# Performance work log

Hardware: AMD Instinct MI355X
Metric: run time of the kernel (lower is better)

Reference implementation:

```python
import jax, jax.numpy as jnp
import numpy as np

B, N, IN, H = 8, 2048, 256, 128
ALPHA = 0.2  # leaky relu slope


def setup_inputs() -> dict:
    key = jax.random.key(0)
    k1, k2, k3, k4 = jax.random.split(key, 4)
    x = jax.random.normal(k1, (B, N, IN), dtype=jnp.float32)
    # adj_identity: batched identity matrix (masks self-attention, then re-adds weight-1 self loop)
    adj_identity = jnp.broadcast_to(jnp.eye(N, dtype=jnp.float32), (B, N, N))
    W = jax.random.normal(k2, (H, IN), dtype=jnp.float32) * (1.0 / np.sqrt(IN))
    b = jnp.zeros((H,), dtype=jnp.float32)
    # atten_fact: [2H, 1], xavier_normal with gain=1.414
    std = 1.414 * np.sqrt(2.0 / (2 * H + 1))
    a = jax.random.normal(k3, (2 * H, 1), dtype=jnp.float32) * std
    return {"input": x, "adj_identity": adj_identity, "W": W, "b": b, "a": a}


def reference(input, adj_identity, W, b, a):
    # input projection: [B,N,H]
    h = jnp.einsum("bni,hi->bnh", input, W) + b
    # decomposition of cat([h_i, h_j]) @ a == h_i@a1 + h_j@a2 (exact same math,
    # avoids materializing the [B, N*N, 2H] tensor)
    a1 = a[:H, 0]  # [H]
    a2 = a[H:, 0]  # [H]
    si = h @ a1  # [B,N]
    sj = h @ a2  # [B,N]
    scores = jax.nn.leaky_relu(si[:, :, None] + sj[:, None, :], negative_slope=ALPHA)  # [B,N,N]
    scores = jnp.where(adj_identity != 0, -jnp.inf, scores)
    attn = jax.nn.softmax(scores, axis=-1) + adj_identity  # [B,N,N]
    # dropout p=0.0 -> identity
    out = jax.nn.elu(jnp.einsum("bnm,bmh->bnh", attn, h))
    return out
```

## Files before the change

### kernel.cpp

```cpp
#include <hip/hip_runtime.h>
#include <hip/hip_bf16.h>
#include <cmath>


#define ALPHA 0.2f
#define NN 2048
#define NIN 256
#define NH 128

typedef __attribute__((ext_vector_type(8))) short short8;
typedef __attribute__((ext_vector_type(4))) float f32x4;

__device__ __forceinline__ unsigned int pk2(float a, float b) {
    unsigned int r;
    asm("v_cvt_pk_bf16_f32 %0, %1, %2" : "=v"(r) : "v"(a), "v"(b));
    return r;
}

__global__ __launch_bounds__(256) void k1_h(
    const float* __restrict__ x, const float* __restrict__ Wm,
    const float* __restrict__ bias, const float* __restrict__ av,
    float* __restrict__ si, float* __restrict__ sj,
    unsigned short* __restrict__ hTt)
{
    __shared__ __align__(16) unsigned short xls[64 * 264];
    __shared__ __align__(16) unsigned short Wls[128 * 264];
    __shared__ float a1l[128], a2l[128], bl[128];

    const int t = threadIdx.x;
    const int r0 = blockIdx.x * 64;

    for (int p = 0; p < 16; ++p) {
        int idx = p * 256 + t;
        int row = idx >> 6, kq = idx & 63;
        f32x4 v = *(const f32x4*)(x + (size_t)(r0 + row) * NIN + kq * 4);
        *(uint2*)(&xls[row * 264 + kq * 4]) = make_uint2(pk2(v[0], v[1]), pk2(v[2], v[3]));
    }
    for (int p = 0; p < 32; ++p) {
        int idx = p * 256 + t;
        int row = idx >> 6, kq = idx & 63;
        f32x4 v = *(const f32x4*)(Wm + (size_t)row * NIN + kq * 4);
        *(uint2*)(&Wls[row * 264 + kq * 4]) = make_uint2(pk2(v[0], v[1]), pk2(v[2], v[3]));
    }
    if (t < 128) { a1l[t] = av[t]; a2l[t] = av[128 + t]; bl[t] = bias[t]; }
    __syncthreads();

    const int w = t >> 6, l = t & 63, la = l & 15, g = l >> 4;

    f32x4 acc[8];
#pragma unroll
    for (int n = 0; n < 8; ++n) acc[n] = (f32x4){0.f, 0.f, 0.f, 0.f};

#pragma unroll
    for (int ks = 0; ks < 8; ++ks) {
        short8 af = *(const short8*)(&xls[(w * 16 + la) * 264 + ks * 32 + g * 8]);
#pragma unroll
        for (int n = 0; n < 8; ++n) {
            short8 bfr = *(const short8*)(&Wls[(n * 16 + la) * 264 + ks * 32 + g * 8]);
            acc[n] = __builtin_amdgcn_mfma_f32_16x16x32_bf16(af, bfr, acc[n], 0, 0, 0);
        }
    }

    float s1[4] = {0.f, 0.f, 0.f, 0.f}, s2[4] = {0.f, 0.f, 0.f, 0.f};
#pragma unroll
    for (int n = 0; n < 8; ++n) {
        int col = n * 16 + la;
#pragma unroll
        for (int r = 0; r < 4; ++r) {
            float v = acc[n][r] + bl[col];
            acc[n][r] = v;
            s1[r] += v * a1l[col];
            s2[r] += v * a2l[col];
        }
    }
#pragma unroll
    for (int r = 0; r < 4; ++r) {
#pragma unroll
        for (int m = 1; m < 16; m <<= 1) {
            s1[r] += __shfl_xor(s1[r], m, 64);
            s2[r] += __shfl_xor(s2[r], m, 64);
        }
    }
    if (la == 0) {
#pragma unroll
        for (int r = 0; r < 4; ++r) {
            int row = w * 16 + g * 4 + r;
            si[r0 + row] = s1[r];
            sj[r0 + row] = s2[r];
        }
    }

    __syncthreads();
    unsigned short* oT = xls;
#pragma unroll
    for (int n = 0; n < 8; ++n) {
        int col = n * 16 + la;
        int row0 = w * 16 + g * 4;
        *(uint2*)(&oT[col * 72 + row0]) =
            make_uint2(pk2(acc[n][0], acc[n][1]), pk2(acc[n][2], acc[n][3]));
    }
    __syncthreads();
    const int b = r0 >> 11, jt = (r0 & (NN - 1)) >> 6;
    unsigned short* dst = hTt + ((size_t)(b * 32 + jt)) * 8192;
    for (int p = 0; p < 4; ++p) {
        int idx = p * 256 + t;
        int col = idx >> 3, seg = idx & 7;
        uint4 v = *(const uint4*)(&oT[col * 72 + seg * 8]);
        *(uint4*)(dst + col * 64 + seg * 8) = v;
    }
}

__global__ __launch_bounds__(512) void k3_attn(
    const unsigned short* __restrict__ hTt,
    const float* __restrict__ si, const float* __restrict__ sj,
    float* __restrict__ out)
{
    __shared__ __align__(16) float f1l[NN];
    __shared__ __align__(16) float f2l[NN];
    __shared__ __align__(16) unsigned short hl[2][128 * 72];
    __shared__ float Zl[2][64];
    __shared__ float mr1[8], mr2[8];

    const int t = threadIdx.x;
    const int bb = blockIdx.x >> 5;
    const int i0 = (blockIdx.x & 31) * 64;
    const int w = t >> 6, l = t & 63;
    const int wr = w >> 2;
    const int wcg = (w >> 1) & 1;
    const int wk = w & 1;
    const int la = l & 15, g = l >> 4;

    const unsigned short* tb = hTt + (size_t)bb * (32 * 8192);

    uint4 c0 = ((const uint4*)tb)[t];
    uint4 c1 = ((const uint4*)tb)[t + 512];

    ((f32x4*)f1l)[t] = ((const f32x4*)(sj + bb * NN))[t];
    __syncthreads();
    f32x4 vv = ((const f32x4*)f1l)[t];
    float m1, m2;
    {
        float hi0 = fmaxf(vv[0], vv[1]), lo0 = fminf(vv[0], vv[1]);
        float hi1 = fmaxf(vv[2], vv[3]), lo1 = fminf(vv[2], vv[3]);
        m1 = fmaxf(hi0, hi1);
        m2 = fmaxf(fminf(hi0, hi1), fmaxf(lo0, lo1));
    }
#pragma unroll
    for (int m = 1; m < 64; m <<= 1) {
        float o1 = __shfl_xor(m1, m, 64), o2 = __shfl_xor(m2, m, 64);
        float n1 = fmaxf(m1, o1);
        float n2 = fmaxf(fminf(m1, o1), fmaxf(m2, o2));
        m1 = n1; m2 = n2;
    }
    if (l == 0) { mr1[w] = m1; mr2[w] = m2; }
    __syncthreads();
    {
        float a1 = mr1[0], a2 = mr2[0];
#pragma unroll
        for (int wv2 = 1; wv2 < 8; ++wv2) {
            float b1 = mr1[wv2], b2 = mr2[wv2];
            float n1 = fmaxf(a1, b1), n2 = fmaxf(fminf(a1, b1), fmaxf(a2, b2));
            a1 = n1; a2 = n2;
        }
        m1 = a1; m2 = a2;
    }
    {
        f32x4 e1t, e2t;
#pragma unroll
        for (int u = 0; u < 4; ++u) { e1t[u] = expf(vv[u]); e2t[u] = expf(ALPHA * vv[u]); }
        ((f32x4*)f1l)[t] = e1t;
        ((f32x4*)f2l)[t] = e2t;
    }

    float e1v[2], e2v[2], owv[2];
#pragma unroll
    for (int fr = 0; fr < 2; ++fr) {
        int gi = bb * NN + i0 + wr * 32 + fr * 16 + la;
        float svi = si[gi], svj = sj[gi];
        float M = (svj == m1) ? m2 : m1;
        float sm = svi + M;
        float mm = sm > 0.f ? sm : ALPHA * sm;
        float a = expf(svi - mm), b2 = expf(ALPHA * svi - mm);
        e1v[fr] = a; e2v[fr] = b2;
        float owr = fmaxf(a * expf(svj), b2 * expf(ALPHA * svj));
        owv[fr] = __uint_as_float(pk2(owr, owr) << 16);
    }

    f32x4 acc[2][4], zac[2];
#pragma unroll
    for (int fr = 0; fr < 2; ++fr) {
        zac[fr] = (f32x4){0.f, 0.f, 0.f, 0.f};
#pragma unroll
        for (int n = 0; n < 4; ++n) acc[fr][n] = (f32x4){0.f, 0.f, 0.f, 0.f};
    }
    short8 ones;
#pragma unroll
    for (int u = 0; u < 8; ++u) ones[u] = (short)0x3F80;

    const int sidx0 = (t >> 3) * 72 + (t & 7) * 8;
    const int sidx1 = ((t + 512) >> 3) * 72 + (t & 7) * 8;

    for (int jt = 0; jt < 32; ++jt) {
        unsigned short* buf = hl[jt & 1];
        *(uint4*)(&buf[sidx0]) = c0;
        *(uint4*)(&buf[sidx1]) = c1;
        if (jt < 31) {
            const uint4* nt = (const uint4*)(tb + (size_t)(jt + 1) * 8192);
            c0 = nt[t];
            c1 = nt[t + 512];
        }
        __syncthreads();

        const int jb = jt * 64 + wk * 32 + g * 8;
        f32x4 F1a = *(const f32x4*)(f1l + jb);
        f32x4 F1b = *(const f32x4*)(f1l + jb + 4);
        f32x4 F2a = *(const f32x4*)(f2l + jb);
        f32x4 F2b = *(const f32x4*)(f2l + jb + 4);

        short8 af[2];
#pragma unroll
        for (int fr = 0; fr < 2; ++fr) {
            const float e1 = e1v[fr], e2 = e2v[fr];
            float w0 = fmaxf(e1 * F1a[0], e2 * F2a[0]);
            float w1 = fmaxf(e1 * F1a[1], e2 * F2a[1]);
            float w2 = fmaxf(e1 * F1a[2], e2 * F2a[2]);
            float w3 = fmaxf(e1 * F1a[3], e2 * F2a[3]);
            float w4 = fmaxf(e1 * F1b[0], e2 * F2b[0]);
            float w5 = fmaxf(e1 * F1b[1], e2 * F2b[1]);
            float w6 = fmaxf(e1 * F1b[2], e2 * F2b[2]);
            float w7 = fmaxf(e1 * F1b[3], e2 * F2b[3]);
            union { unsigned int u[4]; short8 s; } cv;
            cv.u[0] = pk2(w0, w1);
            cv.u[1] = pk2(w2, w3);
            cv.u[2] = pk2(w4, w5);
            cv.u[3] = pk2(w6, w7);
            af[fr] = cv.s;
        }
#pragma unroll
        for (int n = 0; n < 4; ++n) {
            const int col = wcg * 64 + n * 16 + la;
            short8 bfr = *(const short8*)(&buf[col * 72 + wk * 32 + g * 8]);
            acc[0][n] = __builtin_amdgcn_mfma_f32_16x16x32_bf16(af[0], bfr, acc[0][n], 0, 0, 0);
            acc[1][n] = __builtin_amdgcn_mfma_f32_16x16x32_bf16(af[1], bfr, acc[1][n], 0, 0, 0);
        }
        zac[0] = __builtin_amdgcn_mfma_f32_16x16x32_bf16(af[0], ones, zac[0], 0, 0, 0);
        zac[1] = __builtin_amdgcn_mfma_f32_16x16x32_bf16(af[1], ones, zac[1], 0, 0, 0);
    }

    __syncthreads();
    float* xch = (float*)hl;
    const int pair = wr * 2 + wcg;
    if (wk == 1) {
#pragma unroll
        for (int fr = 0; fr < 2; ++fr)
#pragma unroll
            for (int n = 0; n < 4; ++n)
#pragma unroll
                for (int r = 0; r < 4; ++r)
                    xch[(fr * 16 + n * 4 + r) * 256 + pair * 64 + l] = acc[fr][n][r];
    }
    if (wcg == 0 && la == 0) {
#pragma unroll
        for (int fr = 0; fr < 2; ++fr)
#pragma unroll
            for (int r = 0; r < 4; ++r)
                Zl[wk][wr * 32 + fr * 16 + g * 4 + r] = zac[fr][r];
    }
    __syncthreads();

    if (wk == 0) {
#pragma unroll
        for (int fr = 0; fr < 2; ++fr)
#pragma unroll
            for (int n = 0; n < 4; ++n)
#pragma unroll
                for (int r = 0; r < 4; ++r)
                    acc[fr][n][r] += xch[(fr * 16 + n * 4 + r) * 256 + pair * 64 + l];

#pragma unroll
        for (int fr = 0; fr < 2; ++fr) {
#pragma unroll
            for (int n = 0; n < 4; ++n) {
                const int col = wcg * 64 + n * 16 + la;
#pragma unroll
                for (int r = 0; r < 4; ++r) {
                    const int row = wr * 32 + fr * 16 + g * 4 + r;
                    const float Z = Zl[0][row] + Zl[1][row];
                    const int srcl = (g * 4 + r) | (l & 48);
                    const float owq = __shfl(owv[fr], srcl, 64);
                    const float hv = __uint_as_float(
                        (unsigned int)tb[(i0 >> 6) * 8192 + col * 64 + row] << 16);
                    const float num = acc[fr][n][r] - owq * hv;
                    const float den = Z - owq;
                    float o = num / den + hv;
                    out[(size_t)(bb * NN + i0 + row) * NH + col] = o > 0.f ? o : expm1f(o);
                }
            }
        }
    }
}

extern "C" void kernel_launch(void* const* d_in, const int* in_sizes, int n_in,
                              void* d_out, int out_size, void* d_ws, size_t ws_size,
                              hipStream_t stream)
{
    const float* x    = (const float*)d_in[0];
    const float* Wm   = (const float*)d_in[2];
    const float* bias = (const float*)d_in[3];
    const float* av   = (const float*)d_in[4];
    float* out = (float*)d_out;

    float* wsf = (float*)d_ws;
    unsigned short* hTt = (unsigned short*)wsf;
    float* si = wsf + 1048576;
    float* sj = wsf + 1064960;

    hipLaunchKernelGGL(k1_h,    dim3(256), dim3(256), 0, stream, x, Wm, bias, av, si, sj, hTt);
    hipLaunchKernelGGL(k3_attn, dim3(256), dim3(512), 0, stream, hTt, si, sj, out);
}
```

Before: 42.31 us.

## Load B fragments directly from global in MFMA layout and split K across waves

Changes the hTt workspace layout so each lane can load its MFMA B-fragment directly from global memory as a short8. This removes the LDS staging buffer and the per-tile __syncthreads from the attention loop. Waves now cover all 64 rows (4 fragments) and split the key dimension four ways (two halves times two k-slices), with software prefetch two tiles ahead. The partial sums are reduced through a shared exchange buffer in three serialized rounds, and the blockIdx mapping is swizzled so batch varies fastest. The cost is more registers per wave, more global loads that are partly redundant across waves, and a longer reduction at the end.

```diff
diff --git a/kernel.cpp b/kernel.cpp
--- a/kernel.cpp
+++ b/kernel.cpp
@@ -103,10 +103,10 @@
     const int b = r0 >> 11, jt = (r0 & (NN - 1)) >> 6;
     unsigned short* dst = hTt + ((size_t)(b * 32 + jt)) * 8192;
     for (int p = 0; p < 4; ++p) {
-        int idx = p * 256 + t;
-        int col = idx >> 3, seg = idx & 7;
+        int q = p * 256 + t;
+        int col = q & 127, seg = q >> 7;
         uint4 v = *(const uint4*)(&oT[col * 72 + seg * 8]);
-        *(uint4*)(dst + col * 64 + seg * 8) = v;
+        *(uint4*)(dst + q * 8) = v;
     }
 }
 
@@ -117,27 +117,32 @@
 {
     __shared__ __align__(16) float f1l[NN];
     __shared__ __align__(16) float f2l[NN];
-    __shared__ __align__(16) unsigned short hl[2][128 * 72];
-    __shared__ float Zl[2][64];
+    __shared__ __align__(16) float xch[64][128];
+    __shared__ float Zl[4][64];
     __shared__ float mr1[8], mr2[8];
 
     const int t = threadIdx.x;
-    const int bb = blockIdx.x >> 5;
-    const int i0 = (blockIdx.x & 31) * 64;
+    const int bb = blockIdx.x & 7;
+    const int grp = blockIdx.x >> 3;
+    const int i0 = grp * 64;
     const int w = t >> 6, l = t & 63;
-    const int wr = w >> 2;
-    const int wcg = (w >> 1) & 1;
-    const int wk = w & 1;
+    const int wcg = w >> 2;
+    const int dup = (w >> 1) & 1;
+    const int wk  = w & 1;
     const int la = l & 15, g = l >> 4;
+    const int dw = dup * 2 + wk;
 
     const unsigned short* tb = hTt + (size_t)bb * (32 * 8192);
-
-    uint4 c0 = ((const uint4*)tb)[t];
-    uint4 c1 = ((const uint4*)tb)[t + 512];
-
-    ((f32x4*)f1l)[t] = ((const f32x4*)(sj + bb * NN))[t];
-    __syncthreads();
-    f32x4 vv = ((const f32x4*)f1l)[t];
+    const unsigned short* bp = tb + (size_t)dup * (16 * 8192)
+                             + ((wk * 4 + g) * 128 + wcg * 64 + la) * 8;
+
+    short8 Pc[4], Pn[4];
+#pragma unroll
+    for (int n = 0; n < 4; ++n) Pc[n] = *(const short8*)(bp + n * 128);
+#pragma unroll
+    for (int n = 0; n < 4; ++n) Pn[n] = *(const short8*)(bp + 8192 + n * 128);
+
+    f32x4 vv = ((const f32x4*)(sj + bb * NN))[t];
     float m1, m2;
     {
         float hi0 = fmaxf(vv[0], vv[1]), lo0 = fminf(vv[0], vv[1]);
@@ -172,10 +177,10 @@
         ((f32x4*)f2l)[t] = e2t;
     }
 
-    float e1v[2], e2v[2], owv[2];
-#pragma unroll
-    for (int fr = 0; fr < 2; ++fr) {
-        int gi = bb * NN + i0 + wr * 32 + fr * 16 + la;
+    float e1v[4], e2v[4], owv[4];
+#pragma unroll
+    for (int fr = 0; fr < 4; ++fr) {
+        int gi = bb * NN + i0 + fr * 16 + la;
         float svi = si[gi], svj = sj[gi];
         float M = (svj == m1) ? m2 : m1;
         float sm = svi + M;
@@ -185,10 +190,11 @@
         float owr = fmaxf(a * expf(svj), b2 * expf(ALPHA * svj));
         owv[fr] = __uint_as_float(pk2(owr, owr) << 16);
     }
-
-    f32x4 acc[2][4], zac[2];
-#pragma unroll
-    for (int fr = 0; fr < 2; ++fr) {
+    __syncthreads();
+
+    f32x4 acc[4][4], zac[4];
+#pragma unroll
+    for (int fr = 0; fr < 4; ++fr) {
         zac[fr] = (f32x4){0.f, 0.f, 0.f, 0.f};
 #pragma unroll
         for (int n = 0; n < 4; ++n) acc[fr][n] = (f32x4){0.f, 0.f, 0.f, 0.f};
@@ -197,29 +203,17 @@
 #pragma unroll
     for (int u = 0; u < 8; ++u) ones[u] = (short)0x3F80;
 
-    const int sidx0 = (t >> 3) * 72 + (t & 7) * 8;
-    const int sidx1 = ((t + 512) >> 3) * 72 + (t & 7) * 8;
-
-    for (int jt = 0; jt < 32; ++jt) {
-        unsigned short* buf = hl[jt & 1];
-        *(uint4*)(&buf[sidx0]) = c0;
-        *(uint4*)(&buf[sidx1]) = c1;
-        if (jt < 31) {
-            const uint4* nt = (const uint4*)(tb + (size_t)(jt + 1) * 8192);
-            c0 = nt[t];
-            c1 = nt[t + 512];
-        }
-        __syncthreads();
-
-        const int jb = jt * 64 + wk * 32 + g * 8;
+    const int jb0 = dup * 1024 + wk * 32 + g * 8;
+
+#pragma unroll 2
+    for (int s = 0; s < 16; ++s) {
+        const int jb = jb0 + s * 64;
         f32x4 F1a = *(const f32x4*)(f1l + jb);
         f32x4 F1b = *(const f32x4*)(f1l + jb + 4);
         f32x4 F2a = *(const f32x4*)(f2l + jb);
         f32x4 F2b = *(const f32x4*)(f2l + jb + 4);
-
-        short8 af[2];
-#pragma unroll
-        for (int fr = 0; fr < 2; ++fr) {
+#pragma unroll
+        for (int fr = 0; fr < 4; ++fr) {
             const float e1 = e1v[fr], e2 = e2v[fr];
             float w0 = fmaxf(e1 * F1a[0], e2 * F2a[0]);
             float w1 = fmaxf(e1 * F1a[1], e2 * F2a[1]);
@@ -229,71 +223,79 @@
             float w5 = fmaxf(e1 * F1b[1], e2 * F2b[1]);
             float w6 = fmaxf(e1 * F1b[2], e2 * F2b[2]);
             float w7 = fmaxf(e1 * F1b[3], e2 * F2b[3]);
-            union { unsigned int u[4]; short8 s; } cv;
-            cv.u[0] = pk2(w0, w1);
-            cv.u[1] = pk2(w2, w3);
-            cv.u[2] = pk2(w4, w5);
-            cv.u[3] = pk2(w6, w7);
-            af[fr] = cv.s;
-        }
-#pragma unroll
-        for (int n = 0; n < 4; ++n) {
-            const int col = wcg * 64 + n * 16 + la;
-            short8 bfr = *(const short8*)(&buf[col * 72 + wk * 32 + g * 8]);
-            acc[0][n] = __builtin_amdgcn_mfma_f32_16x16x32_bf16(af[0], bfr, acc[0][n], 0, 0, 0);
-            acc[1][n] = __builtin_amdgcn_mfma_f32_16x16x32_bf16(af[1], bfr, acc[1][n], 0, 0, 0);
-        }
-        zac[0] = __builtin_amdgcn_mfma_f32_16x16x32_bf16(af[0], ones, zac[0], 0, 0, 0);
-        zac[1] = __builtin_amdgcn_mfma_f32_16x16x32_bf16(af[1], ones, zac[1], 0, 0, 0);
-    }
-
-    __syncthreads();
-    float* xch = (float*)hl;
-    const int pair = wr * 2 + wcg;
-    if (wk == 1) {
-#pragma unroll
-        for (int fr = 0; fr < 2; ++fr)
-#pragma unroll
-            for (int n = 0; n < 4; ++n)
-#pragma unroll
-                for (int r = 0; r < 4; ++r)
-                    xch[(fr * 16 + n * 4 + r) * 256 + pair * 64 + l] = acc[fr][n][r];
-    }
+            union { unsigned int u4[4]; short8 s8; } cv;
+            cv.u4[0] = pk2(w0, w1);
+            cv.u4[1] = pk2(w2, w3);
+            cv.u4[2] = pk2(w4, w5);
+            cv.u4[3] = pk2(w6, w7);
+            const short8 af = cv.s8;
+            acc[fr][0] = __builtin_amdgcn_mfma_f32_16x16x32_bf16(af, Pc[0], acc[fr][0], 0, 0, 0);
+            acc[fr][1] = __builtin_amdgcn_mfma_f32_16x16x32_bf16(af, Pc[1], acc[fr][1], 0, 0, 0);
+            acc[fr][2] = __builtin_amdgcn_mfma_f32_16x16x32_bf16(af, Pc[2], acc[fr][2], 0, 0, 0);
+            acc[fr][3] = __builtin_amdgcn_mfma_f32_16x16x32_bf16(af, Pc[3], acc[fr][3], 0, 0, 0);
+            zac[fr]   = __builtin_amdgcn_mfma_f32_16x16x32_bf16(af, ones, zac[fr], 0, 0, 0);
+        }
+#pragma unroll
+        for (int n = 0; n < 4; ++n) Pc[n] = Pn[n];
+        if (s + 2 < 16) {
+            const unsigned short* np = bp + (size_t)(s + 2) * 8192;
+#pragma unroll
+            for (int n = 0; n < 4; ++n) Pn[n] = *(const short8*)(np + n * 128);
+        }
+    }
+
     if (wcg == 0 && la == 0) {
 #pragma unroll
-        for (int fr = 0; fr < 2; ++fr)
+        for (int fr = 0; fr < 4; ++fr)
 #pragma unroll
             for (int r = 0; r < 4; ++r)
-                Zl[wk][wr * 32 + fr * 16 + g * 4 + r] = zac[fr][r];
-    }
-    __syncthreads();
-
-    if (wk == 0) {
-#pragma unroll
-        for (int fr = 0; fr < 2; ++fr)
-#pragma unroll
-            for (int n = 0; n < 4; ++n)
-#pragma unroll
-                for (int r = 0; r < 4; ++r)
-                    acc[fr][n][r] += xch[(fr * 16 + n * 4 + r) * 256 + pair * 64 + l];
-
-#pragma unroll
-        for (int fr = 0; fr < 2; ++fr) {
+                Zl[dw][fr * 16 + g * 4 + r] = zac[fr][r];
+    }
+
+#pragma unroll
+    for (int k = 1; k <= 3; ++k) {
+        if (k > 1) __syncthreads();
+        if (dw == k) {
+#pragma unroll
+            for (int fr = 0; fr < 4; ++fr)
+#pragma unroll
+                for (int n = 0; n < 4; ++n)
+#pragma unroll
+                    for (int r = 0; r < 4; ++r)
+                        xch[fr * 16 + n * 4 + r][wcg * 64 + l] = acc[fr][n][r];
+        }
+        __syncthreads();
+        if (dw == 0) {
+#pragma unroll
+            for (int fr = 0; fr < 4; ++fr)
+#pragma unroll
+                for (int n = 0; n < 4; ++n)
+#pragma unroll
+                    for (int r = 0; r < 4; ++r)
+                        acc[fr][n][r] += xch[fr * 16 + n * 4 + r][wcg * 64 + l];
+        }
+    }
+
+    if (dw == 0) {
+#pragma unroll
+        for (int fr = 0; fr < 4; ++fr) {
 #pragma unroll
             for (int n = 0; n < 4; ++n) {
                 const int col = wcg * 64 + n * 16 + la;
 #pragma unroll
                 for (int r = 0; r < 4; ++r) {
-                    const int row = wr * 32 + fr * 16 + g * 4 + r;
-                    const float Z = Zl[0][row] + Zl[1][row];
+                    const int row = fr * 16 + g * 4 + r;
+                    const float Z = Zl[0][row] + Zl[1][row] + Zl[2][row] + Zl[3][row];
                     const int srcl = (g * 4 + r) | (l & 48);
                     const float owq = __shfl(owv[fr], srcl, 64);
+                    const int gRow = i0 + row;
+                    const int jt_r = gRow >> 6, jin = gRow & 63;
                     const float hv = __uint_as_float(
-                        (unsigned int)tb[(i0 >> 6) * 8192 + col * 64 + row] << 16);
+                        (unsigned int)tb[jt_r * 8192 + ((jin >> 3) * 128 + col) * 8 + (jin & 7)] << 16);
                     const float num = acc[fr][n][r] - owq * hv;
                     const float den = Z - owq;
                     float o = num / den + hv;
-                    out[(size_t)(bb * NN + i0 + row) * NH + col] = o > 0.f ? o : expm1f(o);
+                    out[(size_t)(bb * NN + gRow) * NH + col] = o > 0.f ? o : expm1f(o);
                 }
             }
         }
```

After: 41.94 us. Within noise of the previous version (-0.9%).
